# Performance work log

Hardware: AMD Instinct MI355X
Metric: run time of the kernel (lower is better)

## Reference

```python
import jax, jax.numpy as jnp
import numpy as np

NEG = -1e30  # finite stand-in for -inf so softmax grads stay clean


def setup_inputs() -> dict:
    key = jax.random.key(0)
    k1, k2 = jax.random.split(key)
    C, D = 8192, 512
    gt_class_embeddings = jax.random.normal(k1, (C, D), dtype=jnp.float32)
    w = jax.random.normal(k2, (C, D), dtype=jnp.float32)
    return {"gt_class_embeddings": gt_class_embeddings, "w": w}


def reference(gt_class_embeddings, w):
    # L2-normalize class embeddings, cosine-similarity matrix S (diag == 1)
    G = gt_class_embeddings / jnp.linalg.norm(gt_class_embeddings, axis=-1, keepdims=True)
    S = G @ G.T  # [C, C]
    C = S.shape[0]
    off_diag = ~jnp.eye(C, dtype=bool)

    # seSoftmax: per-row softmax over entries != 1 (off-diagonal); diagonal stays 1
    P = jax.nn.softmax(jnp.where(off_diag, S, NEG), axis=-1)
    S2 = jnp.where(off_diag, P, 1.0)

    # argsort(-S2)[1] == most similar (diag value 1 always ranks first),
    # argsort(-S2)[-1] == least similar == row min (softmax values < 1)
    ms = jnp.argmax(jnp.where(off_diag, S2, NEG), axis=-1)  # [C]
    ls = jnp.argmin(jnp.where(off_diag, S2, -NEG), axis=-1)  # [C]

    rows = jnp.arange(C)
    margin = S2[rows, ms] - S2[rows, ls]  # [C]

    d_ms = jnp.sqrt(jnp.sum((w - w[ms]) ** 2, axis=-1))  # [C]
    d_ls = jnp.sqrt(jnp.sum((w - w[ls]) ** 2, axis=-1))  # [C]

    loss = jnp.mean(jnp.maximum(0.0, d_ms - d_ls + margin))
    return loss
```

## Files before the change

kernel.cpp:

```cpp
#include <hip/hip_runtime.h>
#include <math.h>

#define CDIM 8192
#define DDIM 512
#define NEGF -3.0e38f
#define POSF  3.0e38f

#define BM 128
#define NSLOT (CDIM / BM)

typedef __attribute__((ext_vector_type(8))) short bf16x8;
typedef __attribute__((ext_vector_type(4))) float f32x4;

__device__ __forceinline__ unsigned short f2bf(float x) {
    unsigned int u = __float_as_uint(x);
    u += 0x7fffu + ((u >> 16) & 1u);
    return (unsigned short)(u >> 16);
}
__device__ __forceinline__ float bf2f(unsigned short h) {
    return __uint_as_float(((unsigned int)h) << 16);
}
__device__ __forceinline__ void gld16(const void* g, void* l) {
    __builtin_amdgcn_global_load_lds(
        (__attribute__((address_space(1))) void*)(void*)g,
        (__attribute__((address_space(3))) void*)l, 16, 0, 0);
}

__global__ __launch_bounds__(256) void k_prep(const float* __restrict__ g,
                                              unsigned short* __restrict__ hi,
                                              unsigned short* __restrict__ lo) {
    const int wave = threadIdx.x >> 6;
    const int lane = threadIdx.x & 63;
    const int row = blockIdx.x * 4 + wave;
    const float4* src = (const float4*)(g + (size_t)row * DDIM);
    const float4 a = src[lane * 2];
    const float4 b = src[lane * 2 + 1];
    float s = a.x * a.x + a.y * a.y + a.z * a.z + a.w * a.w +
              b.x * b.x + b.y * b.y + b.z * b.z + b.w * b.w;
#pragma unroll
    for (int m = 1; m < 64; m <<= 1) s += __shfl_xor(s, m, 64);
    const float rn = rsqrtf(s);
    const float y[8] = {a.x * rn, a.y * rn, a.z * rn, a.w * rn,
                        b.x * rn, b.y * rn, b.z * rn, b.w * rn};
    unsigned int hv[4], lv[4];
#pragma unroll
    for (int i = 0; i < 4; ++i) {
        const unsigned short h0 = f2bf(y[2 * i]);
        const unsigned short h1 = f2bf(y[2 * i + 1]);
        const unsigned short l0 = f2bf(y[2 * i] - bf2f(h0));
        const unsigned short l1 = f2bf(y[2 * i + 1] - bf2f(h1));
        hv[i] = (unsigned int)h0 | ((unsigned int)h1 << 16);
        lv[i] = (unsigned int)l0 | ((unsigned int)l1 << 16);
    }
    uint4* dh = (uint4*)(hi + (size_t)row * DDIM + lane * 8);
    uint4* dl = (uint4*)(lo + (size_t)row * DDIM + lane * 8);
    *dh = make_uint4(hv[0], hv[1], hv[2], hv[3]);
    *dl = make_uint4(lv[0], lv[1], lv[2], lv[3]);
}

__device__ __constant__ unsigned char OSUP[28] = {
    1, 2, 10,   3, 11, 19,   4, 12, 20,   28, 5, 13,
    21, 29, 37, 6,   14, 22, 30, 38,   46, 7, 15, 23,   31, 39, 47, 55};

__global__ __launch_bounds__(256, 3) void k_simstats(
    const unsigned short* __restrict__ ghi, const unsigned short* __restrict__ glo,
    float* __restrict__ pmax, float* __restrict__ pmin, float* __restrict__ pZ,
    int* __restrict__ pamax, int* __restrict__ pamin) {
    const int bid = blockIdx.x;
    const int xcd = bid & 7;
    const int off = bid >> 3;
    int I, J;
    if (xcd < 4) {
        if (off < 72) {
            const int s = xcd * 2 + (off >= 36);
            const int u = (off >= 36) ? off - 36 : off;
            int jj = 0;
            while ((jj + 1) * (jj + 2) / 2 <= u) ++jj;
            const int ii = u - jj * (jj + 1) / 2;
            I = s * 8 + ii; J = s * 8 + jj;
        } else {
            const int sup = (off - 72) >> 6;
            const int u = (off - 72) & 63;
            const int code = OSUP[xcd * 3 + sup];
            I = (code >> 3) * 8 + (u & 7);
            J = (code & 7) * 8 + (u >> 3);
        }
    } else {
        if (off >= 256) return;
        const int sup = off >> 6;
        const int u = off & 63;
        const int code = OSUP[12 + (xcd - 4) * 4 + sup];
        I = (code >> 3) * 8 + (u & 7);
        J = (code & 7) * 8 + (u >> 3);
    }

    __shared__ unsigned short SH[4 * BM * 32];
    unsigned short* Ahi = SH;
    unsigned short* Alo = SH + 4096;
    unsigned short* Bhi = SH + 8192;
    unsigned short* Blo = SH + 12288;
    const int t = threadIdx.x;
    const int wave = t >> 6;
    const int lane = t & 63;
    const int lanelo = lane & 15;
    const int quad = lane >> 4;
    const int wr = wave & 1;
    const int wc = wave >> 1;

    const int srow = t >> 2;
    const int scolb = ((t & 3) ^ ((t >> 3) & 3)) << 4;
    char* lAh = (char*)Ahi + t * 16;
    char* lAl = (char*)Alo + t * 16;
    char* lBh = (char*)Bhi + t * 16;
    char* lBl = (char*)Blo + t * 16;

    const int fsl = (quad ^ ((lanelo >> 1) & 3)) << 3;
    const int aoff = (wr * 64 + lanelo) * 32 + fsl;
    const int boff = (wc * 64 + lanelo) * 32 + fsl;

    float* rm  = (float*)SH;
    float* rz  = rm + 256;
    float* rmn = rz + 256;
    int*   ra  = (int*)(rmn + 256);
    int*   ran = ra + 256;
    float* cm  = (float*)Bhi;
    float* cz  = cm + 256;
    float* cmn = cz + 256;
    int*   ca  = (int*)(cmn + 256);
    int*   can = ca + 256;

    const int i0 = I * BM;
    const int j0 = J * BM;
    const bool isdiag = (I == J);

    f32x4 acc[4][4];
#pragma unroll
    for (int rt = 0; rt < 4; ++rt)
#pragma unroll
        for (int ct = 0; ct < 4; ++ct)
            acc[rt][ct] = (f32x4){0.f, 0.f, 0.f, 0.f};

    const char* baseAh = (const char*)ghi + (size_t)(i0 + srow) * 1024 + scolb;
    const char* baseAl = (const char*)glo + (size_t)(i0 + srow) * 1024 + scolb;
    const char* baseBh = (const char*)ghi + (size_t)(j0 + srow) * 1024 + scolb;
    const char* baseBl = (const char*)glo + (size_t)(j0 + srow) * 1024 + scolb;

    for (int k0 = 0; k0 < DDIM; k0 += 32) {
        __syncthreads();
#pragma unroll
        for (int q = 0; q < 2; ++q) {
            const size_t roff = (size_t)q * 64 * 1024 + k0 * 2;
            gld16(baseAh + roff, lAh + q * 4096);
            gld16(baseAl + roff, lAl + q * 4096);
            gld16(baseBh + roff, lBh + q * 4096);
            gld16(baseBl + roff, lBl + q * 4096);
        }
        __syncthreads();
        bf16x8 ah[4], al[4];
#pragma unroll
        for (int rt = 0; rt < 4; ++rt) {
            ah[rt] = *(const bf16x8*)&Ahi[aoff + rt * 512];
            al[rt] = *(const bf16x8*)&Alo[aoff + rt * 512];
        }
#pragma unroll
        for (int ct = 0; ct < 4; ++ct) {
            const bf16x8 bh = *(const bf16x8*)&Bhi[boff + ct * 512];
            const bf16x8 bl = *(const bf16x8*)&Blo[boff + ct * 512];
#pragma unroll
            for (int rt = 0; rt < 4; ++rt) {
                acc[rt][ct] = __builtin_amdgcn_mfma_f32_16x16x32_bf16(
                    ah[rt], bh, acc[rt][ct], 0, 0, 0);
                acc[rt][ct] = __builtin_amdgcn_mfma_f32_16x16x32_bf16(
                    ah[rt], bl, acc[rt][ct], 0, 0, 0);
                acc[rt][ct] = __builtin_amdgcn_mfma_f32_16x16x32_bf16(
                    al[rt], bh, acc[rt][ct], 0, 0, 0);
            }
        }
    }

    __syncthreads();

#pragma unroll
    for (int rt = 0; rt < 4; ++rt) {
#pragma unroll
        for (int r = 0; r < 4; ++r) {
            const int lrow = wr * 64 + rt * 16 + quad * 4 + r;
            float tmax = NEGF; int targ = 0;
            float tmin = POSF; int targn = 0;
            if (isdiag) {
                const int gi = i0 + lrow;
#pragma unroll
                for (int ct = 0; ct < 4; ++ct) {
                    const int gj = j0 + wc * 64 + ct * 16 + lanelo;
                    const float v = acc[rt][ct][r];
                    const bool dg = (gj == gi);
                    const float vM = dg ? NEGF : v;
                    const float vm = dg ? POSF : v;
                    if (vM > tmax) { tmax = vM; targ = gj; }
                    if (vm < tmin) { tmin = vm; targn = gj; }
                }
            } else {
#pragma unroll
                for (int ct = 0; ct < 4; ++ct) {
                    const int gj = j0 + wc * 64 + ct * 16 + lanelo;
                    const float v = acc[rt][ct][r];
                    if (v > tmax) { tmax = v; targ = gj; }
                    if (v < tmin) { tmin = v; targn = gj; }
                }
            }
#pragma unroll
            for (int msk = 1; msk < 16; msk <<= 1) {
                const float v2 = __shfl_xor(tmax, msk, 64);
                const int i2 = __shfl_xor(targ, msk, 64);
                if (v2 > tmax) { tmax = v2; targ = i2; }
                const float v3 = __shfl_xor(tmin, msk, 64);
                const int i3 = __shfl_xor(targn, msk, 64);
                if (v3 < tmin) { tmin = v3; targn = i3; }
            }
            if (lanelo == 0) {
                const int o = wc * 128 + lrow;
                rm[o] = tmax; rmn[o] = tmin;
                ra[o] = targ; ran[o] = targn;
            }
        }
    }

    if (!isdiag) {
#pragma unroll
        for (int ct = 0; ct < 4; ++ct) {
            const int lcol = wc * 64 + ct * 16 + lanelo;
            float tmax = NEGF; int targ = 0;
            float tmin = POSF; int targn = 0;
#pragma unroll
            for (int rt = 0; rt < 4; ++rt)
#pragma unroll
                for (int r = 0; r < 4; ++r) {
                    const int gi = i0 + wr * 64 + rt * 16 + quad * 4 + r;
                    const float v = acc[rt][ct][r];
                    if (v > tmax) { tmax = v; targ = gi; }
                    if (v < tmin) { tmin = v; targn = gi; }
                }
#pragma unroll
            for (int msk = 16; msk < 64; msk <<= 1) {
                const float m2 = __shfl_xor(tmax, msk, 64);
                const int i2 = __shfl_xor(targ, msk, 64);
                if (m2 > tmax) { tmax = m2; targ = i2; }
                const float mn2 = __shfl_xor(tmin, msk, 64);
                const int in2 = __shfl_xor(targn, msk, 64);
                if (mn2 < tmin) { tmin = mn2; targn = in2; }
            }
            if (quad == 0) {
                const int o = wr * 128 + lcol;
                cm[o] = tmax; cmn[o] = tmin;
                ca[o] = targ; can[o] = targn;
            }
        }
    }

#pragma unroll
    for (int rt = 0; rt < 4; ++rt)
#pragma unroll
        for (int ct = 0; ct < 4; ++ct)
#pragma unroll
            for (int r = 0; r < 4; ++r)
                acc[rt][ct][r] = __expf(acc[rt][ct][r] - 1.f);
    if (isdiag && wr == wc) {
#pragma unroll
        for (int rt = 0; rt < 4; ++rt)
#pragma unroll
            for (int r = 0; r < 4; ++r)
                if (lanelo == quad * 4 + r) acc[rt][rt][r] = 0.f;
    }

#pragma unroll
    for (int rt = 0; rt < 4; ++rt)
#pragma unroll
        for (int r = 0; r < 4; ++r) {
            float s = acc[rt][0][r] + acc[rt][1][r] +
                      acc[rt][2][r] + acc[rt][3][r];
#pragma unroll
            for (int msk = 1; msk < 16; msk <<= 1) s += __shfl_xor(s, msk, 64);
            if (lanelo == 0)
                rz[wc * 128 + wr * 64 + rt * 16 + quad * 4 + r] = s;
        }

    if (!isdiag) {
#pragma unroll
        for (int ct = 0; ct < 4; ++ct) {
            float s = 0.f;
#pragma unroll
            for (int rt = 0; rt < 4; ++rt)
                s += acc[rt][ct][0] + acc[rt][ct][1] +
                     acc[rt][ct][2] + acc[rt][ct][3];
#pragma unroll
            for (int msk = 16; msk < 64; msk <<= 1) s += __shfl_xor(s, msk, 64);
            if (quad == 0)
                cz[wr * 128 + wc * 64 + ct * 16 + lanelo] = s;
        }
    }

    __syncthreads();

    if (t < BM) {
        const float m0 = rm[t], m1 = rm[128 + t];
        float vmax = m0; int imax = ra[t];
        if (m1 > vmax) { vmax = m1; imax = ra[128 + t]; }
        float vmin = rmn[t]; int imin = ran[t];
        if (rmn[128 + t] < vmin) { vmin = rmn[128 + t]; imin = ran[128 + t]; }
        const size_t o = (size_t)J * CDIM + i0 + t;
        pmax[o] = vmax; pmin[o] = vmin; pZ[o] = rz[t] + rz[128 + t];
        pamax[o] = imax; pamin[o] = imin;
    } else if (!isdiag) {
        const int tt = t - BM;
        const float m0 = cm[tt], m1 = cm[128 + tt];
        float vmax = m0; int imax = ca[tt];
        if (m1 > vmax) { vmax = m1; imax = ca[128 + tt]; }
        float vmin = cmn[tt]; int imin = can[tt];
        if (cmn[128 + tt] < vmin) { vmin = cmn[128 + tt]; imin = can[128 + tt]; }
        const size_t o = (size_t)I * CDIM + j0 + tt;
        pmax[o] = vmax; pmin[o] = vmin; pZ[o] = cz[tt] + cz[128 + tt];
        pamax[o] = imax; pamin[o] = imin;
    }
}

__global__ __launch_bounds__(256) void k_merge(
    const float* __restrict__ pmax, const float* __restrict__ pmin,
    const float* __restrict__ pZ, const int* __restrict__ pamax,
    const int* __restrict__ pamin, float* __restrict__ margin,
    int* __restrict__ ms, int* __restrict__ ls) {
    const int row = blockIdx.x * 256 + threadIdx.x;
    float M = NEGF; int a = 0;
    float mn = POSF; int b = 0;
    float Z = 0.f;
    for (int s = 0; s < NSLOT; ++s) {
        const size_t o = (size_t)s * CDIM + row;
        const float v = pmax[o];
        const int ia = pamax[o];
        const float u = pmin[o];
        const int ib = pamin[o];
        Z += pZ[o];
        if (v > M) { M = v; a = ia; }
        if (u < mn) { mn = u; b = ib; }
    }
    margin[row] = (1.f - __expf(mn - M)) * __expf(M - 1.f) / Z;
    ms[row] = a;
    ls[row] = b;
}

__global__ __launch_bounds__(256) void k_dist(
    const float* __restrict__ w, const float* __restrict__ margin,
    const int* __restrict__ ms, const int* __restrict__ ls,
    float* __restrict__ vals) {
    const int wave = threadIdx.x >> 6;
    const int lane = threadIdx.x & 63;
    const int row = blockIdx.x * 4 + wave;
    const int jm = ms[row], jl = ls[row];
    const float4* wi = (const float4*)(w + (size_t)row * DDIM);
    const float4* wm = (const float4*)(w + (size_t)jm * DDIM);
    const float4* wl = (const float4*)(w + (size_t)jl * DDIM);
    float sm = 0.f, sl = 0.f;
#pragma unroll
    for (int h = 0; h < 2; ++h) {
        const int idx = h * 64 + lane;
        const float4 x = wi[idx];
        const float4 y = wm[idx];
        const float4 c = wl[idx];
        float d;
        d = x.x - y.x; sm = fmaf(d, d, sm);
        d = x.y - y.y; sm = fmaf(d, d, sm);
        d = x.z - y.z; sm = fmaf(d, d, sm);
        d = x.w - y.w; sm = fmaf(d, d, sm);
        d = x.x - c.x; sl = fmaf(d, d, sl);
        d = x.y - c.y; sl = fmaf(d, d, sl);
        d = x.z - c.z; sl = fmaf(d, d, sl);
        d = x.w - c.w; sl = fmaf(d, d, sl);
    }
#pragma unroll
    for (int msk = 1; msk < 64; msk <<= 1) {
        sm += __shfl_xor(sm, msk, 64);
        sl += __shfl_xor(sl, msk, 64);
    }
    if (lane == 0) {
        const float val = sqrtf(sm) - sqrtf(sl) + margin[row];
        vals[row] = val > 0.f ? val : 0.f;
    }
}

__global__ __launch_bounds__(256) void k_final(const float* __restrict__ vals,
                                               float* __restrict__ out) {
    __shared__ float red[256];
    float s = 0.f;
    for (int i = threadIdx.x; i < CDIM; i += 256) s += vals[i];
    red[threadIdx.x] = s;
    __syncthreads();
#pragma unroll
    for (int k = 128; k > 0; k >>= 1) {
        if (threadIdx.x < (unsigned)k) red[threadIdx.x] += red[threadIdx.x + k];
        __syncthreads();
    }
    if (threadIdx.x == 0) out[0] = red[0] * (1.0f / CDIM);
}

extern "C" void kernel_launch(void* const* d_in, const int* in_sizes, int n_in,
                              void* d_out, int out_size, void* d_ws, size_t ws_size,
                              hipStream_t stream) {
    const float* g = (const float*)d_in[0];
    const float* w = (const float*)d_in[1];
    float* out = (float*)d_out;

    unsigned short* ghi = (unsigned short*)d_ws;
    unsigned short* glo = ghi + (size_t)CDIM * DDIM;
    float* p = (float*)(glo + (size_t)CDIM * DDIM);
    float* pmax = p;      p += (size_t)NSLOT * CDIM;
    float* pmin = p;      p += (size_t)NSLOT * CDIM;
    float* pZ = p;        p += (size_t)NSLOT * CDIM;
    int* pamax = (int*)p; p += (size_t)NSLOT * CDIM;
    int* pamin = (int*)p; p += (size_t)NSLOT * CDIM;
    float* vals = p;      p += CDIM;
    float* margin = p;    p += CDIM;
    int* ms = (int*)p;    p += CDIM;
    int* ls = (int*)p;    p += CDIM;

    k_prep<<<CDIM / 4, 256, 0, stream>>>(g, ghi, glo);
    k_simstats<<<2112, 256, 0, stream>>>(ghi, glo, pmax, pmin, pZ, pamax, pamin);
    k_merge<<<CDIM / 256, 256, 0, stream>>>(pmax, pmin, pZ, pamax, pamin,
                                            margin, ms, ls);
    k_dist<<<CDIM / 4, 256, 0, stream>>>(w, margin, ms, ls, vals);
    k_final<<<1, 256, 0, stream>>>(vals, out);
}
```

Baseline: 244.7 us.

## Fuse slot merge into distance kernel and raise simstats occupancy bound

```diff
diff --git a/kernel.cpp b/kernel.cpp
--- a/kernel.cpp
+++ b/kernel.cpp
@@ -62,7 +62,7 @@
     1, 2, 10,   3, 11, 19,   4, 12, 20,   28, 5, 13,
     21, 29, 37, 6,   14, 22, 30, 38,   46, 7, 15, 23,   31, 39, 47, 55};
 
-__global__ __launch_bounds__(256, 3) void k_simstats(
+__global__ __launch_bounds__(256, 4) void k_simstats(
     const unsigned short* __restrict__ ghi, const unsigned short* __restrict__ glo,
     float* __restrict__ pmax, float* __restrict__ pmin, float* __restrict__ pZ,
     int* __restrict__ pamax, int* __restrict__ pamin) {
@@ -323,38 +323,31 @@
     }
 }
 
-__global__ __launch_bounds__(256) void k_merge(
+__global__ __launch_bounds__(256) void k_lossc(
     const float* __restrict__ pmax, const float* __restrict__ pmin,
     const float* __restrict__ pZ, const int* __restrict__ pamax,
-    const int* __restrict__ pamin, float* __restrict__ margin,
-    int* __restrict__ ms, int* __restrict__ ls) {
-    const int row = blockIdx.x * 256 + threadIdx.x;
-    float M = NEGF; int a = 0;
-    float mn = POSF; int b = 0;
-    float Z = 0.f;
-    for (int s = 0; s < NSLOT; ++s) {
-        const size_t o = (size_t)s * CDIM + row;
-        const float v = pmax[o];
-        const int ia = pamax[o];
-        const float u = pmin[o];
-        const int ib = pamin[o];
-        Z += pZ[o];
-        if (v > M) { M = v; a = ia; }
-        if (u < mn) { mn = u; b = ib; }
-    }
-    margin[row] = (1.f - __expf(mn - M)) * __expf(M - 1.f) / Z;
-    ms[row] = a;
-    ls[row] = b;
-}
-
-__global__ __launch_bounds__(256) void k_dist(
-    const float* __restrict__ w, const float* __restrict__ margin,
-    const int* __restrict__ ms, const int* __restrict__ ls,
+    const int* __restrict__ pamin, const float* __restrict__ w,
     float* __restrict__ vals) {
     const int wave = threadIdx.x >> 6;
     const int lane = threadIdx.x & 63;
     const int row = blockIdx.x * 4 + wave;
-    const int jm = ms[row], jl = ls[row];
+    const size_t o = (size_t)lane * CDIM + row;
+    float v = pmax[o]; int a = pamax[o];
+    float u = pmin[o]; int b = pamin[o];
+    float z = pZ[o];
+#pragma unroll
+    for (int msk = 1; msk < 64; msk <<= 1) {
+        const float v2 = __shfl_xor(v, msk, 64);
+        const int i2 = __shfl_xor(a, msk, 64);
+        if (v2 > v) { v = v2; a = i2; }
+        const float v3 = __shfl_xor(u, msk, 64);
+        const int i3 = __shfl_xor(b, msk, 64);
+        if (v3 < u) { u = v3; b = i3; }
+        z += __shfl_xor(z, msk, 64);
+    }
+    const float margin = (1.f - __expf(u - v)) * __expf(v - 1.f) / z;
+    const int jm = a, jl = b;
+
     const float4* wi = (const float4*)(w + (size_t)row * DDIM);
     const float4* wm = (const float4*)(w + (size_t)jm * DDIM);
     const float4* wl = (const float4*)(w + (size_t)jl * DDIM);
@@ -381,7 +374,7 @@
         sl += __shfl_xor(sl, msk, 64);
     }
     if (lane == 0) {
-        const float val = sqrtf(sm) - sqrtf(sl) + margin[row];
+        const float val = sqrtf(sm) - sqrtf(sl) + margin;
         vals[row] = val > 0.f ? val : 0.f;
     }
 }
@@ -417,14 +410,9 @@
     int* pamax = (int*)p; p += (size_t)NSLOT * CDIM;
     int* pamin = (int*)p; p += (size_t)NSLOT * CDIM;
     float* vals = p;      p += CDIM;
-    float* margin = p;    p += CDIM;
-    int* ms = (int*)p;    p += CDIM;
-    int* ls = (int*)p;    p += CDIM;
 
     k_prep<<<CDIM / 4, 256, 0, stream>>>(g, ghi, glo);
     k_simstats<<<2112, 256, 0, stream>>>(ghi, glo, pmax, pmin, pZ, pamax, pamin);
-    k_merge<<<CDIM / 256, 256, 0, stream>>>(pmax, pmin, pZ, pamax, pamin,
-                                            margin, ms, ls);
-    k_dist<<<CDIM / 4, 256, 0, stream>>>(w, margin, ms, ls, vals);
+    k_lossc<<<CDIM / 4, 256, 0, stream>>>(pmax, pmin, pZ, pamax, pamin, w, vals);
     k_final<<<1, 256, 0, stream>>>(vals, out);
 }
```

Measured after the change: 328.8 us. 34.4% more time.
